# Performance work log

Hardware: AMD Instinct MI355X
Metric: run time of the kernel (lower is better)

Reference implementation:

```python
import jax, jax.numpy as jnp
import numpy as np

WIDTH = 32
DEPTH = 4
N_NODES = 50000
N_EDGES = 1600000


def setup_inputs() -> dict:
    key = jax.random.key(0)
    ks = jax.random.split(key, 10)
    N, E, W = N_NODES, N_EDGES, WIDTH
    s = 0.1
    x = jax.random.normal(ks[0], (N, 3), dtype=jnp.float32)
    edge_index = jax.random.randint(ks[1], (2, E), 0, N, dtype=jnp.int64)
    edge_attr = jax.random.uniform(ks[2], (E, 3), dtype=jnp.float32)
    # fc1: Linear(3, W); fc2: Linear(W, 1)
    fc1_w = jax.random.normal(ks[3], (W, 3), dtype=jnp.float32) * s
    fc1_b = jnp.zeros((W,), jnp.float32)
    fc2_w = jax.random.normal(ks[4], (1, W), dtype=jnp.float32) * s
    fc2_b = jnp.zeros((1,), jnp.float32)
    # 3 structurally distinct NNConv layers (reused DEPTH times), stacked on axis 0.
    # Edge-kernel MLP: Linear(3, W//4) -> ReLU -> Linear(W//4, W)
    kw1 = jax.random.normal(ks[5], (3, W // 4, 3), dtype=jnp.float32) * s
    kb1 = jnp.zeros((3, W // 4), jnp.float32)
    kw2 = jax.random.normal(ks[6], (3, W, W // 4), dtype=jnp.float32) * s
    kb2 = jnp.zeros((3, W), jnp.float32)
    # NNConv root weight [in, out] and bias
    root = jax.random.normal(ks[7], (3, W, W), dtype=jnp.float32) * s
    cbias = jnp.zeros((3, W), jnp.float32)
    return {"x": x, "edge_index": edge_index, "edge_attr": edge_attr,
            "fc1_w": fc1_w, "fc1_b": fc1_b, "fc2_w": fc2_w, "fc2_b": fc2_b,
            "kw1": kw1, "kb1": kb1, "kw2": kw2, "kb2": kb2,
            "root": root, "cbias": cbias}


def reference(x, edge_index, edge_attr, fc1_w, fc1_b, fc2_w, fc2_b,
              kw1, kb1, kw2, kb2, root, cbias):
    N = x.shape[0]
    src, dst = edge_index[0], edge_index[1]
    # in-degree counts for scatter-mean (clamped to 1 like PyG)
    counts = jax.ops.segment_sum(jnp.ones(dst.shape[0], x.dtype), dst, num_segments=N)
    inv_counts = 1.0 / jnp.maximum(counts, 1.0)

    h = x @ fc1_w.T + fc1_b  # [N, W]
    for _ in range(DEPTH):
        for c in range(3):
            # diagonal NNConv: edge MLP -> per-edge weight vector [E, W]
            w = jax.nn.relu(edge_attr @ kw1[c].T + kb1[c]) @ kw2[c].T + kb2[c]
            msg = h[src] * w                      # gather + elementwise per-edge product
            agg = jax.ops.segment_sum(msg, dst, num_segments=N) * inv_counts[:, None]
            h = jax.nn.relu(agg + h @ root[c] + cbias[c])
    return h @ fc2_w.T + fc2_b  # [N, 1]
```

## Files before the change

### kernel.cpp

```cpp
#include <hip/hip_runtime.h>

#define WN 32
#define HID 8
#define DEPTH 4
#define GPB 16

typedef float fvec4 __attribute__((ext_vector_type(4)));

__global__ void zero_kernel(int* __restrict__ cnt, int* __restrict__ cursor, int n) {
    int i = blockIdx.x * blockDim.x + threadIdx.x;
    if (i < n) { cnt[i] = 0; cursor[i] = 0; }
}

__global__ void count_kernel(const int* __restrict__ eidx, int* __restrict__ cnt, int e_cnt) {
    int e = blockIdx.x * blockDim.x + threadIdx.x;
    if (e >= e_cnt) return;
    atomicAdd(&cnt[eidx[e_cnt + e]], 1);
}

__global__ void scan_kernel(const int* __restrict__ cnt, int* __restrict__ row_ptr,
                            float* __restrict__ inv, int n) {
    __shared__ int s_wave[16];
    int t = threadIdx.x;
    int lane = t & 63;
    int wv = t >> 6;
    int offset = 0;
    for (int base = 0; base < n; base += 1024) {
        int i = base + t;
        int v = (i < n) ? cnt[i] : 0;
        int x = v;
#pragma unroll
        for (int d = 1; d < 64; d <<= 1) {
            int y = __shfl_up(x, d, 64);
            if (lane >= d) x += y;
        }
        if (lane == 63) s_wave[wv] = x;
        __syncthreads();
        if (wv == 0 && lane < 16) {
            int y = s_wave[lane];
#pragma unroll
            for (int d = 1; d < 16; d <<= 1) {
                int z = __shfl_up(y, d, 64);
                if (lane >= d) y += z;
            }
            s_wave[lane] = y;
        }
        __syncthreads();
        int waveoff = (wv > 0) ? s_wave[wv - 1] : 0;
        int total = s_wave[15];
        int incl = x + waveoff + offset;
        if (i < n) {
            row_ptr[i + 1] = incl;
            inv[i] = 1.0f / (float)(v > 1 ? v : 1);
        }
        offset += total;
        __syncthreads();
    }
    if (t == 0) row_ptr[0] = 0;
}

__global__ void scatter_kernel(const int* __restrict__ eidx, const float* __restrict__ ea,
                               const int* __restrict__ row_ptr, int* __restrict__ cursor,
                               fvec4* __restrict__ rec, int e_cnt) {
    int e = blockIdx.x * blockDim.x + threadIdx.x;
    if (e >= e_cnt) return;
    int src = eidx[e];
    int dst = eidx[e_cnt + e];
    int pos = row_ptr[dst] + atomicAdd(&cursor[dst], 1);
    fvec4 r;
    r.x = __int_as_float(src);
    r.y = ea[3 * e];
    r.z = ea[3 * e + 1];
    r.w = ea[3 * e + 2];
    rec[pos] = r;
}

__global__ void h0_kernel(const float* __restrict__ x, const float* __restrict__ fc1_w,
                          const float* __restrict__ fc1_b, float* __restrict__ h, int n) {
    __shared__ float s_w[WN * 3];
    __shared__ float s_b[WN];
    int t = threadIdx.x;
    if (t < WN * 3) s_w[t] = fc1_w[t];
    if (t < WN) s_b[t] = fc1_b[t];
    __syncthreads();
    int i = blockIdx.x * blockDim.x + t;
    if (i >= n) return;
    float x0 = x[3 * i], x1 = x[3 * i + 1], x2 = x[3 * i + 2];
#pragma unroll
    for (int j = 0; j < WN; j++) {
        h[(size_t)i * WN + j] = s_b[j] + s_w[j * 3] * x0 + s_w[j * 3 + 1] * x1 + s_w[j * 3 + 2] * x2;
    }
}

__global__ void gather2_kernel(const int* __restrict__ row_ptr, const fvec4* __restrict__ rec,
                               const float* __restrict__ h_in, float* __restrict__ h_out,
                               const float* __restrict__ inv,
                               const float* __restrict__ kw1, const float* __restrict__ kb1,
                               const float* __restrict__ kw2, const float* __restrict__ kb2,
                               const float* __restrict__ root, const float* __restrict__ cbias,
                               int n) {
    __shared__ float s_root[WN * 34];
    __shared__ float s_h[GPB * 34];
    __shared__ int   s_src[GPB][33];
    __shared__ fvec4 s_hid_u[GPB][33];
    __shared__ fvec4 s_hid_v[GPB][33];
    __shared__ int   s_maxdeg;

    int t = threadIdx.x;
    if (t == 0) s_maxdeg = 0;
    for (int i = t; i < WN * WN; i += 256) s_root[(i >> 5) * 34 + (i & 31)] = root[i];

    int grp = t >> 4;
    int tc  = t & 15;
    int node = blockIdx.x * GPB + grp;
    bool valid = node < n;

    const fvec4* kwp = (const fvec4*)(kw2 + tc * 16);
    fvec4 wa0 = kwp[0], wa1 = kwp[1];
    fvec4 wb0 = kwp[2], wb1 = kwp[3];
    float2 b2 = *(const float2*)(kb2 + 2 * tc);
    float2 cb = *(const float2*)(cbias + 2 * tc);

    int e0 = 0, e1 = 0;
    float2 hself = {0.0f, 0.0f};
    if (valid) {
        e0 = row_ptr[node];
        e1 = row_ptr[node + 1];
        hself = *(const float2*)(h_in + (size_t)node * WN + 2 * tc);
    }
    *(float2*)&s_h[grp * 34 + 2 * tc] = hself;
    int deg = e1 - e0;
    __syncthreads();
    if (valid && tc == 0 && deg > 0) atomicMax(&s_maxdeg, deg);
    __syncthreads();
    int nchunk = (s_maxdeg + 31) >> 5;

    float acc0 = 0.0f, acc1 = 0.0f;
    for (int cs = 0; cs < nchunk; cs++) {
        int ebase = e0 + (cs << 5);
#pragma unroll
        for (int s = 0; s < 2; s++) {
            int li = tc + (s << 4);
            int e = ebase + li;
            if (e < e1) {
                fvec4 r = rec[e];
                s_src[grp][li] = __float_as_int(r.x);
                float hv[HID];
#pragma unroll
                for (int j = 0; j < HID; j++) {
                    float u = kb1[j] + kw1[3 * j] * r.y + kw1[3 * j + 1] * r.z + kw1[3 * j + 2] * r.w;
                    hv[j] = u > 0.0f ? u : 0.0f;
                }
                fvec4 lo, hi;
                lo.x = hv[0]; lo.y = hv[1]; lo.z = hv[2]; lo.w = hv[3];
                hi.x = hv[4]; hi.y = hv[5]; hi.z = hv[6]; hi.w = hv[7];
                s_hid_u[grp][li] = lo;
                s_hid_v[grp][li] = hi;
            }
        }
        __syncthreads();
        int rem = e1 - ebase;
        int cnt = rem < 32 ? rem : 32;
#pragma unroll 4
        for (int i = 0; i < cnt; i++) {
            int src = s_src[grp][i];
            fvec4 u = s_hid_u[grp][i];
            fvec4 v = s_hid_v[grp][i];
            float w0 = b2.x + wa0.x * u.x + wa0.y * u.y + wa0.z * u.z + wa0.w * u.w
                            + wa1.x * v.x + wa1.y * v.y + wa1.z * v.z + wa1.w * v.w;
            float w1 = b2.y + wb0.x * u.x + wb0.y * u.y + wb0.z * u.z + wb0.w * u.w
                            + wb1.x * v.x + wb1.y * v.y + wb1.z * v.z + wb1.w * v.w;
            float2 hh = *(const float2*)(h_in + (size_t)src * WN + 2 * tc);
            acc0 += hh.x * w0;
            acc1 += hh.y * w1;
        }
        __syncthreads();
    }
    if (!valid) return;

    float invn = inv[node];
    float r0 = acc0 * invn + cb.x;
    float r1 = acc1 * invn + cb.y;
#pragma unroll
    for (int k = 0; k < WN; k++) {
        float hk = s_h[grp * 34 + k];
        float2 rt = *(const float2*)&s_root[k * 34 + 2 * tc];
        r0 += hk * rt.x;
        r1 += hk * rt.y;
    }
    float2 o;
    o.x = r0 > 0.0f ? r0 : 0.0f;
    o.y = r1 > 0.0f ? r1 : 0.0f;
    *(float2*)(h_out + (size_t)node * WN + 2 * tc) = o;
}

__global__ void out_kernel(const float* __restrict__ h, const float* __restrict__ fc2_w,
                           const float* __restrict__ fc2_b, float* __restrict__ out, int n) {
    __shared__ float s_w[WN];
    __shared__ float s_b;
    int t = threadIdx.x;
    if (t < WN) s_w[t] = fc2_w[t];
    if (t == 0) s_b = fc2_b[0];
    __syncthreads();
    int i = blockIdx.x * blockDim.x + t;
    if (i >= n) return;
    float acc = s_b;
#pragma unroll
    for (int k = 0; k < WN; k++) acc += h[(size_t)i * WN + k] * s_w[k];
    out[i] = acc;
}

extern "C" void kernel_launch(void* const* d_in, const int* in_sizes, int n_in,
                              void* d_out, int out_size, void* d_ws, size_t ws_size,
                              hipStream_t stream) {
    const float* x      = (const float*)d_in[0];
    const int*   eidx   = (const int*)d_in[1];
    const float* ea     = (const float*)d_in[2];
    const float* fc1_w  = (const float*)d_in[3];
    const float* fc1_b  = (const float*)d_in[4];
    const float* fc2_w  = (const float*)d_in[5];
    const float* fc2_b  = (const float*)d_in[6];
    const float* kw1    = (const float*)d_in[7];
    const float* kb1    = (const float*)d_in[8];
    const float* kw2    = (const float*)d_in[9];
    const float* kb2    = (const float*)d_in[10];
    const float* root   = (const float*)d_in[11];
    const float* cbias  = (const float*)d_in[12];
    float* out = (float*)d_out;

    const int n = in_sizes[0] / 3;
    const int e_cnt = in_sizes[2] / 3;

    auto pad4 = [](size_t v) { return (v + 3) & ~(size_t)3; };
    float* ws = (float*)d_ws;
    size_t off = 0;
    float* hA       = ws + off; off += pad4((size_t)n * WN);
    float* hB       = ws + off; off += pad4((size_t)n * WN);
    float* inv      = ws + off; off += pad4(n);
    int*   cnt      = (int*)(ws + off); off += pad4(n);
    int*   cursor   = (int*)(ws + off); off += pad4(n);
    int*   row_ptr  = (int*)(ws + off); off += pad4(n + 1);
    fvec4* rec      = (fvec4*)(ws + off); off += (size_t)4 * e_cnt;

    const int B = 256;
    int grid_n  = (n + B - 1) / B;
    int grid_e  = (e_cnt + B - 1) / B;
    int grid_g  = (n + GPB - 1) / GPB;

    zero_kernel<<<grid_n, B, 0, stream>>>(cnt, cursor, n);
    count_kernel<<<grid_e, B, 0, stream>>>(eidx, cnt, e_cnt);
    scan_kernel<<<1, 1024, 0, stream>>>(cnt, row_ptr, inv, n);
    scatter_kernel<<<grid_e, B, 0, stream>>>(eidx, ea, row_ptr, cursor, rec, e_cnt);
    h0_kernel<<<grid_n, B, 0, stream>>>(x, fc1_w, fc1_b, hA, n);

    float* hin = hA;
    float* hout = hB;
    for (int d = 0; d < DEPTH; d++) {
        for (int c = 0; c < 3; c++) {
            gather2_kernel<<<grid_g, B, 0, stream>>>(
                row_ptr, rec, hin, hout, inv,
                kw1 + (size_t)c * HID * 3, kb1 + (size_t)c * HID,
                kw2 + (size_t)c * WN * HID, kb2 + (size_t)c * WN,
                root + (size_t)c * WN * WN, cbias + (size_t)c * WN, n);
            float* tmp = hin; hin = hout; hout = tmp;
        }
    }
    out_kernel<<<grid_n, B, 0, stream>>>(hin, fc2_w, fc2_b, out, n);
}
```

Measured before the change: 764.0 us.

## Record edge ranks during counting and parallelize the CSR prefix scan

The count kernel now saves each edge's atomicAdd return value as its rank within its destination. The scatter step can then place records without a second pass of atomics on a cursor array. The single-block serial scan over all nodes is replaced by a three-stage scan: block sums, a scan over those sums, then per-block local scans. This cuts the atomic traffic and the serial bottleneck of the scan, at the cost of an extra rank array of E ints and two more kernel launches.

```diff
diff --git a/kernel.cpp b/kernel.cpp
--- a/kernel.cpp
+++ b/kernel.cpp
@@ -7,27 +7,39 @@
 
 typedef float fvec4 __attribute__((ext_vector_type(4)));
 
-__global__ void zero_kernel(int* __restrict__ cnt, int* __restrict__ cursor, int n) {
+__global__ void zero_kernel(int* __restrict__ cnt, int n) {
     int i = blockIdx.x * blockDim.x + threadIdx.x;
-    if (i < n) { cnt[i] = 0; cursor[i] = 0; }
-}
-
-__global__ void count_kernel(const int* __restrict__ eidx, int* __restrict__ cnt, int e_cnt) {
+    if (i < n) cnt[i] = 0;
+}
+
+__global__ void rank_kernel(const int* __restrict__ eidx, int* __restrict__ cnt,
+                            int* __restrict__ rank, int e_cnt) {
     int e = blockIdx.x * blockDim.x + threadIdx.x;
     if (e >= e_cnt) return;
-    atomicAdd(&cnt[eidx[e_cnt + e]], 1);
-}
-
-__global__ void scan_kernel(const int* __restrict__ cnt, int* __restrict__ row_ptr,
-                            float* __restrict__ inv, int n) {
-    __shared__ int s_wave[16];
-    int t = threadIdx.x;
-    int lane = t & 63;
-    int wv = t >> 6;
+    rank[e] = atomicAdd(&cnt[eidx[e_cnt + e]], 1);
+}
+
+__global__ void scan1_kernel(const int* __restrict__ cnt, int* __restrict__ blk_sum, int n) {
+    __shared__ int s_wave[4];
+    int t = threadIdx.x;
+    int lane = t & 63, wv = t >> 6;
+    int i = blockIdx.x * 256 + t;
+    int v = (i < n) ? cnt[i] : 0;
+#pragma unroll
+    for (int d = 1; d < 64; d <<= 1) v += __shfl_xor(v, d, 64);
+    if (lane == 0) s_wave[wv] = v;
+    __syncthreads();
+    if (t == 0) blk_sum[blockIdx.x] = s_wave[0] + s_wave[1] + s_wave[2] + s_wave[3];
+}
+
+__global__ void scan2_kernel(const int* __restrict__ blk_sum, int* __restrict__ blk_base, int nblk) {
+    __shared__ int s_wave[4];
+    int t = threadIdx.x;
+    int lane = t & 63, wv = t >> 6;
     int offset = 0;
-    for (int base = 0; base < n; base += 1024) {
+    for (int base = 0; base < nblk; base += 256) {
         int i = base + t;
-        int v = (i < n) ? cnt[i] : 0;
+        int v = (i < nblk) ? blk_sum[i] : 0;
         int x = v;
 #pragma unroll
         for (int d = 1; d < 64; d <<= 1) {
@@ -36,10 +48,10 @@
         }
         if (lane == 63) s_wave[wv] = x;
         __syncthreads();
-        if (wv == 0 && lane < 16) {
+        if (wv == 0 && lane < 4) {
             int y = s_wave[lane];
 #pragma unroll
-            for (int d = 1; d < 16; d <<= 1) {
+            for (int d = 1; d < 4; d <<= 1) {
                 int z = __shfl_up(y, d, 64);
                 if (lane >= d) y += z;
             }
@@ -47,26 +59,54 @@
         }
         __syncthreads();
         int waveoff = (wv > 0) ? s_wave[wv - 1] : 0;
-        int total = s_wave[15];
-        int incl = x + waveoff + offset;
-        if (i < n) {
-            row_ptr[i + 1] = incl;
-            inv[i] = 1.0f / (float)(v > 1 ? v : 1);
-        }
+        int total = s_wave[3];
+        if (i < nblk) blk_base[i] = x + waveoff + offset - v;
         offset += total;
         __syncthreads();
     }
-    if (t == 0) row_ptr[0] = 0;
-}
-
-__global__ void scatter_kernel(const int* __restrict__ eidx, const float* __restrict__ ea,
-                               const int* __restrict__ row_ptr, int* __restrict__ cursor,
-                               fvec4* __restrict__ rec, int e_cnt) {
+}
+
+__global__ void scan3_kernel(const int* __restrict__ cnt, const int* __restrict__ blk_base,
+                             int* __restrict__ row_ptr, float* __restrict__ inv, int n) {
+    __shared__ int s_wave[4];
+    int t = threadIdx.x;
+    int lane = t & 63, wv = t >> 6;
+    int i = blockIdx.x * 256 + t;
+    int v = (i < n) ? cnt[i] : 0;
+    int x = v;
+#pragma unroll
+    for (int d = 1; d < 64; d <<= 1) {
+        int y = __shfl_up(x, d, 64);
+        if (lane >= d) x += y;
+    }
+    if (lane == 63) s_wave[wv] = x;
+    __syncthreads();
+    if (wv == 0 && lane < 4) {
+        int y = s_wave[lane];
+#pragma unroll
+        for (int d = 1; d < 4; d <<= 1) {
+            int z = __shfl_up(y, d, 64);
+            if (lane >= d) y += z;
+        }
+        s_wave[lane] = y;
+    }
+    __syncthreads();
+    int waveoff = (wv > 0) ? s_wave[wv - 1] : 0;
+    if (i < n) {
+        row_ptr[i + 1] = blk_base[blockIdx.x] + waveoff + x;
+        inv[i] = 1.0f / (float)(v > 1 ? v : 1);
+    }
+    if (i == 0) row_ptr[0] = 0;
+}
+
+__global__ void place_kernel(const int* __restrict__ eidx, const float* __restrict__ ea,
+                             const int* __restrict__ row_ptr, const int* __restrict__ rank,
+                             fvec4* __restrict__ rec, int e_cnt) {
     int e = blockIdx.x * blockDim.x + threadIdx.x;
     if (e >= e_cnt) return;
     int src = eidx[e];
     int dst = eidx[e_cnt + e];
-    int pos = row_ptr[dst] + atomicAdd(&cursor[dst], 1);
+    int pos = row_ptr[dst] + rank[e];
     fvec4 r;
     r.x = __int_as_float(src);
     r.y = ea[3 * e];
@@ -238,19 +278,24 @@
     float* hB       = ws + off; off += pad4((size_t)n * WN);
     float* inv      = ws + off; off += pad4(n);
     int*   cnt      = (int*)(ws + off); off += pad4(n);
-    int*   cursor   = (int*)(ws + off); off += pad4(n);
     int*   row_ptr  = (int*)(ws + off); off += pad4(n + 1);
+    int*   blk_sum  = (int*)(ws + off); off += pad4((n + 255) / 256);
+    int*   blk_base = (int*)(ws + off); off += pad4((n + 255) / 256);
+    int*   rank     = (int*)(ws + off); off += pad4(e_cnt);
     fvec4* rec      = (fvec4*)(ws + off); off += (size_t)4 * e_cnt;
 
     const int B = 256;
     int grid_n  = (n + B - 1) / B;
     int grid_e  = (e_cnt + B - 1) / B;
+    int nblk    = (n + 255) / 256;
     int grid_g  = (n + GPB - 1) / GPB;
 
-    zero_kernel<<<grid_n, B, 0, stream>>>(cnt, cursor, n);
-    count_kernel<<<grid_e, B, 0, stream>>>(eidx, cnt, e_cnt);
-    scan_kernel<<<1, 1024, 0, stream>>>(cnt, row_ptr, inv, n);
-    scatter_kernel<<<grid_e, B, 0, stream>>>(eidx, ea, row_ptr, cursor, rec, e_cnt);
+    zero_kernel<<<grid_n, B, 0, stream>>>(cnt, n);
+    rank_kernel<<<grid_e, B, 0, stream>>>(eidx, cnt, rank, e_cnt);
+    scan1_kernel<<<nblk, B, 0, stream>>>(cnt, blk_sum, n);
+    scan2_kernel<<<1, B, 0, stream>>>(blk_sum, blk_base, nblk);
+    scan3_kernel<<<nblk, B, 0, stream>>>(cnt, blk_base, row_ptr, inv, n);
+    place_kernel<<<grid_e, B, 0, stream>>>(eidx, ea, row_ptr, rank, rec, e_cnt);
     h0_kernel<<<grid_n, B, 0, stream>>>(x, fc1_w, fc1_b, hA, n);
 
     float* hin = hA;
```

After: 670.4 us. -12.3%, faster.
